# Kernel optimization log

Hardware: AMD Instinct MI355X
Metric: run time of the kernel (lower is better)

Reference implementation:

```python
import jax, jax.numpy as jnp
import numpy as np

N_NODES = 50000
N_EDGES = 800000
N_GRAPHS = 1024
N_LAYERS = 5
D_IN, D_HID = 32, 128


def setup_inputs() -> dict:
    key = jax.random.key(0)
    ks = jax.random.split(key, 6)
    x = jax.random.normal(ks[0], (N_NODES, D_IN), dtype=jnp.float32)
    edge_index = jax.random.randint(ks[1], (2, N_EDGES), 0, N_NODES, dtype=jnp.int64)
    batch = jnp.sort(jax.random.randint(ks[2], (N_NODES,), 0, N_GRAPHS, dtype=jnp.int64))
    W_embed = jax.random.normal(ks[3], (D_IN, D_HID), dtype=jnp.float32) * (1.0 / np.sqrt(D_IN))
    Ws = jax.random.normal(ks[4], (N_LAYERS, D_HID, D_HID), dtype=jnp.float32) * (1.0 / np.sqrt(D_HID))
    bs = jax.random.normal(ks[5], (N_LAYERS, D_HID), dtype=jnp.float32) * 0.01
    return {"x": x, "edge_index": edge_index, "batch": batch,
            "W_embed": W_embed, "Ws": Ws, "bs": bs}


def reference(x, edge_index, batch, W_embed, Ws, bs):
    src, dst = edge_index[0], edge_index[1]
    h = x @ W_embed  # [N, 128] embedding (bias=False)
    features = [h]
    for i in range(N_LAYERS):
        # GINConv with eps=0 and explicit self-loops:
        # agg = sum_{j in N(i)} h_j + h_i (self-loop); out = Linear((1+eps)*h_i + agg)
        neigh = jax.ops.segment_sum(h[src], dst, num_segments=N_NODES)
        agg = neigh + 2.0 * h  # self-loop contribution + (1+eps)*h, eps=0
        h = agg @ Ws[i] + bs[i]
        features.append(h)
    node_repr = jnp.concatenate(features, axis=-1)  # [N, 6*128]
    graph_repr = jax.ops.segment_sum(node_repr, batch, num_segments=N_GRAPHS)  # [G, 768]
    return graph_repr
```

## Files before the change

kernel.cpp:

```cpp
#include <hip/hip_runtime.h>

#define N_NODES 50000
#define N_EDGES 800000
#define N_GRAPHS 1024
#define N_LAYERS 5
#define D_IN 32
#define D_HID 128

#define NBUCK 256
#define BUCK_NODES 196
#define BUCK_CAP 4096
#define CHUNK 4096
#define NCHUNKS ((N_EDGES + CHUNK - 1) / CHUNK)

typedef __attribute__((ext_vector_type(8))) short bf16x8;
typedef __attribute__((ext_vector_type(4))) float f32x4;


__device__ __forceinline__ float bf_lo(unsigned u) { return __uint_as_float(u << 16); }
__device__ __forceinline__ float bf_hi(unsigned u) { return __uint_as_float(u & 0xffff0000u); }
__device__ __forceinline__ unsigned bf16_rn(float f) {
  unsigned u = __float_as_uint(f);
  return (u + 0x7fffu + ((u >> 16) & 1u)) >> 16;
}
__device__ __forceinline__ unsigned pack_bf16(float a, float b) {
  return bf16_rn(a) | (bf16_rn(b) << 16);
}


__global__ void zero_int_kernel(int* __restrict__ p, int n) {
  int i = blockIdx.x * blockDim.x + threadIdx.x;
  if (i < n) p[i] = 0;
}

__global__ __launch_bounds__(256) void bucket_count_kernel(const int* __restrict__ dst,
                                                           int* __restrict__ bcount) {
  __shared__ int cnt[NBUCK];
  for (int i = threadIdx.x; i < NBUCK; i += 256) cnt[i] = 0;
  __syncthreads();
  const int cb = blockIdx.x * CHUNK;
  const int end = (cb + CHUNK < N_EDGES) ? cb + CHUNK : N_EDGES;
  for (int e = cb + threadIdx.x; e < end; e += 256)
    atomicAdd(&cnt[dst[e] / BUCK_NODES], 1);
  __syncthreads();
  for (int i = threadIdx.x; i < NBUCK; i += 256)
    if (cnt[i]) atomicAdd(&bcount[i], cnt[i]);
}

__global__ __launch_bounds__(256) void bucket_scan_kernel(const int* __restrict__ bcount,
                                                          int* __restrict__ bbase,
                                                          int* __restrict__ gcur) {
  __shared__ int s[NBUCK];
  const int t = threadIdx.x;
  const int v0 = bcount[t];
  s[t] = v0;
  __syncthreads();
  #pragma unroll
  for (int d = 1; d < NBUCK; d <<= 1) {
    int v = (t >= d) ? s[t - d] : 0;
    __syncthreads();
    s[t] += v;
    __syncthreads();
  }
  bbase[t + 1] = s[t];
  if (t == 0) bbase[0] = 0;
  gcur[t] = s[t] - v0;
}

__global__ __launch_bounds__(256) void bucket_scatter_kernel(const int* __restrict__ src,
                                                             const int* __restrict__ dst,
                                                             int* __restrict__ gcur,
                                                             unsigned long long* __restrict__ aux) {
  __shared__ int cnt[NBUCK];
  __shared__ int base_[NBUCK];
  __shared__ int cur[NBUCK];
  for (int i = threadIdx.x; i < NBUCK; i += 256) cnt[i] = 0;
  __syncthreads();
  const int cb = blockIdx.x * CHUNK;
  const int end = (cb + CHUNK < N_EDGES) ? cb + CHUNK : N_EDGES;
  for (int e = cb + threadIdx.x; e < end; e += 256)
    atomicAdd(&cnt[dst[e] / BUCK_NODES], 1);
  __syncthreads();
  for (int i = threadIdx.x; i < NBUCK; i += 256) {
    base_[i] = cnt[i] ? atomicAdd(&gcur[i], cnt[i]) : 0;
    cur[i] = 0;
  }
  __syncthreads();
  for (int e = cb + threadIdx.x; e < end; e += 256) {
    const int d = dst[e];
    const int b = d / BUCK_NODES;
    const int p = base_[b] + atomicAdd(&cur[b], 1);
    aux[p] = ((unsigned long long)(unsigned)d << 32) | (unsigned)src[e];
  }
}

__global__ __launch_bounds__(256) void bucket_csr_kernel(const unsigned long long* __restrict__ aux,
                                                         const int* __restrict__ bbase,
                                                         int* __restrict__ off,
                                                         int* __restrict__ csr) {
  __shared__ int sdeg[NBUCK];
  __shared__ int sscan[NBUCK];
  __shared__ int scur[NBUCK];
  __shared__ int lcsr[BUCK_CAP];
  const int b = blockIdx.x, t = threadIdx.x;
  const int e0 = bbase[b], e1 = bbase[b + 1];
  const int n0 = b * BUCK_NODES;
  const int nN = (N_NODES - n0 < BUCK_NODES) ? (N_NODES - n0) : BUCK_NODES;
  sdeg[t] = 0;
  __syncthreads();
  for (int i = e0 + t; i < e1; i += 256)
    atomicAdd(&sdeg[(int)(aux[i] >> 32) - n0], 1);
  __syncthreads();
  sscan[t] = sdeg[t];
  __syncthreads();
  #pragma unroll
  for (int d = 1; d < NBUCK; d <<= 1) {
    int v = (t >= d) ? sscan[t - d] : 0;
    __syncthreads();
    sscan[t] += v;
    __syncthreads();
  }
  const int exc_t = sscan[t] - sdeg[t];
  __syncthreads();
  sscan[t] = exc_t;
  scur[t] = 0;
  if (t < nN) off[n0 + t] = e0 + exc_t;
  if (b == NBUCK - 1 && t == 0) off[N_NODES] = e1;
  __syncthreads();
  for (int i = e0 + t; i < e1; i += 256) {
    const unsigned long long v = aux[i];
    const int d = (int)(v >> 32) - n0;
    const int pos = sscan[d] + atomicAdd(&scur[d], 1);
    const int s = (int)(unsigned)(v & 0xffffffffu);
    if (pos < BUCK_CAP) lcsr[pos] = s;
    else csr[e0 + pos] = s;
  }
  __syncthreads();
  const int cntAll = e1 - e0;
  const int lim = (cntAll < BUCK_CAP) ? cntAll : BUCK_CAP;
  for (int i = t; i < lim; i += 256) csr[e0 + i] = lcsr[i];
}

__global__ void graph_off_kernel(const int* __restrict__ batch, int* __restrict__ goff) {
  int g = blockIdx.x * blockDim.x + threadIdx.x;
  if (g <= N_GRAPHS) {
    int lo = 0, hi = N_NODES;
    while (lo < hi) { int mid = (lo + hi) >> 1; if (batch[mid] < g) lo = mid + 1; else hi = mid; }
    goff[g] = lo;
  }
}

__global__ void pack_w_kernel(const float* __restrict__ Ws,
                              unsigned short* __restrict__ wb_hi,
                              unsigned short* __restrict__ wb_lo) {
  int idx = blockIdx.x * blockDim.x + threadIdx.x;
  if (idx >= N_LAYERS * 16384) return;
  int layer = idx >> 14;
  int r = idx & 16383;
  int t = r >> 9;
  int lane = (r >> 3) & 63;
  int i = r & 7;
  int nt = t >> 2, kt = t & 3;
  int k = kt * 32 + (lane >> 4) * 8 + i;
  int c = nt * 16 + (lane & 15);
  float f = Ws[(size_t)layer * 16384 + k * D_HID + c];
  unsigned short h = (unsigned short)bf16_rn(f);
  float hf = __uint_as_float(((unsigned)h) << 16);
  unsigned short l = (unsigned short)bf16_rn(f - hf);
  wb_hi[idx] = h;
  wb_lo[idx] = l;
}


__global__ __launch_bounds__(256) void embed_kernel(const float* __restrict__ x,
                                                    const float* __restrict__ W,
                                                    unsigned short* __restrict__ hb) {
  __shared__ float Wl[D_IN * D_HID];
  __shared__ float xl[64 * D_IN];
  for (int i = threadIdx.x; i < D_IN * D_HID; i += 256) Wl[i] = W[i];
  const int base = blockIdx.x * 64;
  const int nThis = (base + 64 <= N_NODES) ? 64 : (N_NODES - base);
  const float4* x4 = reinterpret_cast<const float4*>(x + (size_t)base * D_IN);
  for (int i = threadIdx.x; i < nThis * (D_IN / 4); i += 256)
    reinterpret_cast<float4*>(xl)[i] = x4[i];
  __syncthreads();
  const int c2 = (threadIdx.x & 63) * 2;
  const int sub = threadIdx.x >> 6;
  for (int r = sub; r < nThis; r += 4) {
    float s0 = 0.f, s1 = 0.f;
    #pragma unroll
    for (int k = 0; k < D_IN; ++k) {
      float xv = xl[r * D_IN + k];
      s0 += xv * Wl[k * D_HID + c2];
      s1 += xv * Wl[k * D_HID + c2 + 1];
    }
    *reinterpret_cast<unsigned*>(hb + (size_t)(base + r) * D_HID + c2) = pack_bf16(s0, s1);
  }
}

__global__ __launch_bounds__(256, 6) void gin_layer_kernel(const unsigned short* __restrict__ hb,
                                                           const int* __restrict__ off,
                                                           const int* __restrict__ csr,
                                                           const unsigned short* __restrict__ wb_hi,
                                                           const unsigned short* __restrict__ wb_lo,
                                                           const float* __restrict__ b,
                                                           unsigned short* __restrict__ hbout) {
  __shared__ unsigned atile[16 * 64];
  const int wid = threadIdx.x >> 6;
  const int lane = threadIdx.x & 63;
  const int base_m = blockIdx.x * 16;
  const int q = lane >> 4;
  const int l16 = lane & 15;
  const int r = wid * 4 + q;
  const int node = base_m + r;

  const int e0 = off[node], e1 = off[node + 1];
  const int deg = e1 - e0;

  float s[8];
  {
    const uint4 su = *reinterpret_cast<const uint4*>(hb + (size_t)node * D_HID + l16 * 8);
    const unsigned* sw = reinterpret_cast<const unsigned*>(&su);
    #pragma unroll
    for (int i = 0; i < 4; ++i) {
      s[2 * i]     = 2.f * bf_lo(sw[i]);
      s[2 * i + 1] = 2.f * bf_hi(sw[i]);
    }
  }

  for (int bb = 0; bb < deg; bb += 16) {
    const int epos = e0 + bb + l16;
    const int vidx = (epos < e1) ? csr[epos] : 0;
    #pragma unroll
    for (int half = 0; half < 2; ++half) {
      const int jb = half * 8;
      if (bb + jb < deg) {
        uint4 u[8];
        #pragma unroll
        for (int j = 0; j < 8; ++j) {
          const int idx = __shfl(vidx, (lane & 48) + jb + j, 64);
          u[j] = *reinterpret_cast<const uint4*>(hb + (size_t)idx * D_HID + l16 * 8);
        }
        const int rem = deg - bb - jb;
        #pragma unroll
        for (int j = 0; j < 8; ++j) {
          const float sc = (j < rem) ? 1.f : 0.f;
          const unsigned* uw = reinterpret_cast<const unsigned*>(&u[j]);
          #pragma unroll
          for (int i = 0; i < 4; ++i) {
            s[2 * i]     += sc * bf_lo(uw[i]);
            s[2 * i + 1] += sc * bf_hi(uw[i]);
          }
        }
      }
    }
  }

  {
    uint4 pk;
    unsigned* pw = reinterpret_cast<unsigned*>(&pk);
    #pragma unroll
    for (int i = 0; i < 4; ++i) pw[i] = pack_bf16(s[2 * i], s[2 * i + 1]);
    const int wbase = (l16 * 4) ^ ((r & 7) << 2);
    *reinterpret_cast<uint4*>(&atile[r * 64 + wbase]) = pk;
  }
  __syncthreads();

  const int l15 = lane & 15;
  const int lg = lane >> 4;
  bf16x8 a[4];
  #pragma unroll
  for (int kt = 0; kt < 4; ++kt) {
    const int u32off = l15 * 64 + ((kt * 16 + lg * 4) ^ ((l15 & 7) << 2));
    a[kt] = *reinterpret_cast<const bf16x8*>(&atile[u32off]);
  }
  #pragma unroll
  for (int qq = 0; qq < 2; ++qq) {
    const int nt = wid * 2 + qq;
    f32x4 acc = {0.f, 0.f, 0.f, 0.f};
    #pragma unroll
    for (int kt = 0; kt < 4; ++kt) {
      const int toff = (nt * 4 + kt) * 512 + lane * 8;
      bf16x8 bh = *reinterpret_cast<const bf16x8*>(wb_hi + toff);
      bf16x8 bl = *reinterpret_cast<const bf16x8*>(wb_lo + toff);
      acc = __builtin_amdgcn_mfma_f32_16x16x32_bf16(a[kt], bh, acc, 0, 0, 0);
      acc = __builtin_amdgcn_mfma_f32_16x16x32_bf16(a[kt], bl, acc, 0, 0, 0);
    }
    const int col = nt * 16 + l15;
    const float bcol = b[col];
    #pragma unroll
    for (int i = 0; i < 4; ++i) {
      const int onode = base_m + lg * 4 + i;
      hbout[(size_t)onode * D_HID + col] = (unsigned short)bf16_rn(acc[i] + bcol);
    }
  }
}

__global__ __launch_bounds__(256) void pool6_kernel(const unsigned short* __restrict__ h0,
                                                    const unsigned short* __restrict__ h1,
                                                    const unsigned short* __restrict__ h2,
                                                    const unsigned short* __restrict__ h3,
                                                    const unsigned short* __restrict__ h4,
                                                    const unsigned short* __restrict__ h5,
                                                    const int* __restrict__ goff,
                                                    float* __restrict__ out) {
  const int g = blockIdx.x * 8 + (threadIdx.x >> 5);
  const int t = threadIdx.x & 31;
  if (g >= N_GRAPHS) return;
  const int n0 = goff[g], n1 = goff[g + 1];
  float4 s0 = {0,0,0,0}, s1 = {0,0,0,0}, s2 = {0,0,0,0};
  float4 s3 = {0,0,0,0}, s4 = {0,0,0,0}, s5 = {0,0,0,0};
  for (int n = n0; n < n1; ++n) {
    const size_t o = (size_t)n * D_HID + t * 4;
    uint2 v0 = *reinterpret_cast<const uint2*>(h0 + o);
    uint2 v1 = *reinterpret_cast<const uint2*>(h1 + o);
    uint2 v2 = *reinterpret_cast<const uint2*>(h2 + o);
    uint2 v3 = *reinterpret_cast<const uint2*>(h3 + o);
    uint2 v4 = *reinterpret_cast<const uint2*>(h4 + o);
    uint2 v5 = *reinterpret_cast<const uint2*>(h5 + o);
    s0.x += bf_lo(v0.x); s0.y += bf_hi(v0.x); s0.z += bf_lo(v0.y); s0.w += bf_hi(v0.y);
    s1.x += bf_lo(v1.x); s1.y += bf_hi(v1.x); s1.z += bf_lo(v1.y); s1.w += bf_hi(v1.y);
    s2.x += bf_lo(v2.x); s2.y += bf_hi(v2.x); s2.z += bf_lo(v2.y); s2.w += bf_hi(v2.y);
    s3.x += bf_lo(v3.x); s3.y += bf_hi(v3.x); s3.z += bf_lo(v3.y); s3.w += bf_hi(v3.y);
    s4.x += bf_lo(v4.x); s4.y += bf_hi(v4.x); s4.z += bf_lo(v4.y); s4.w += bf_hi(v4.y);
    s5.x += bf_lo(v5.x); s5.y += bf_hi(v5.x); s5.z += bf_lo(v5.y); s5.w += bf_hi(v5.y);
  }
  float* ob = out + (size_t)g * ((N_LAYERS + 1) * D_HID) + t * 4;
  *reinterpret_cast<float4*>(ob + 0 * D_HID) = s0;
  *reinterpret_cast<float4*>(ob + 1 * D_HID) = s1;
  *reinterpret_cast<float4*>(ob + 2 * D_HID) = s2;
  *reinterpret_cast<float4*>(ob + 3 * D_HID) = s3;
  *reinterpret_cast<float4*>(ob + 4 * D_HID) = s4;
  *reinterpret_cast<float4*>(ob + 5 * D_HID) = s5;
}


extern "C" void kernel_launch(void* const* d_in, const int* in_sizes, int n_in,
                              void* d_out, int out_size, void* d_ws, size_t ws_size,
                              hipStream_t stream) {
  const float* x       = (const float*)d_in[0];
  const int*   edges   = (const int*)d_in[1];
  const int*   src     = edges;
  const int*   dst     = edges + N_EDGES;
  const int*   batch   = (const int*)d_in[2];
  const float* W_embed = (const float*)d_in[3];
  const float* Ws      = (const float*)d_in[4];
  const float* bs      = (const float*)d_in[5];
  float* out = (float*)d_out;

  const size_t HSZ = (size_t)N_NODES * D_HID;
  unsigned short* hb[N_LAYERS + 1];
  hb[0] = (unsigned short*)d_ws;
  for (int l = 1; l <= N_LAYERS; ++l) hb[l] = hb[l - 1] + HSZ;
  unsigned short* wb_hi = hb[N_LAYERS] + HSZ;
  unsigned short* wb_lo = wb_hi + (size_t)N_LAYERS * 16384;
  unsigned long long* aux = (unsigned long long*)(wb_lo + (size_t)N_LAYERS * 16384);
  int*   off    = (int*)(aux + N_EDGES);
  int*   bcount = off + (N_NODES + 1);
  int*   bbase  = bcount + NBUCK;
  int*   gcur   = bbase + (NBUCK + 1);
  int*   csr    = gcur + NBUCK;
  int*   goff   = csr + N_EDGES;

  zero_int_kernel<<<1, 256, 0, stream>>>(bcount, NBUCK);
  bucket_count_kernel<<<NCHUNKS, 256, 0, stream>>>(dst, bcount);
  bucket_scan_kernel<<<1, NBUCK, 0, stream>>>(bcount, bbase, gcur);
  bucket_scatter_kernel<<<NCHUNKS, 256, 0, stream>>>(src, dst, gcur, aux);
  bucket_csr_kernel<<<NBUCK, 256, 0, stream>>>(aux, bbase, off, csr);
  graph_off_kernel<<<(N_GRAPHS + 1 + 255) / 256, 256, 0, stream>>>(batch, goff);

  pack_w_kernel<<<(N_LAYERS * 16384 + 255) / 256, 256, 0, stream>>>(Ws, wb_hi, wb_lo);

  embed_kernel<<<(N_NODES + 63) / 64, 256, 0, stream>>>(x, W_embed, hb[0]);

  for (int l = 0; l < N_LAYERS; ++l) {
    gin_layer_kernel<<<N_NODES / 16, 256, 0, stream>>>(hb[l], off, csr,
                                                       wb_hi + (size_t)l * 16384,
                                                       wb_lo + (size_t)l * 16384,
                                                       bs + (size_t)l * D_HID, hb[l + 1]);
  }

  pool6_kernel<<<N_GRAPHS / 8, 256, 0, stream>>>(hb[0], hb[1], hb[2], hb[3], hb[4], hb[5],
                                                 goff, out);
}
```

Before: 269.1 us.

## Fuse pooling into layer epilogues via atomics and drop CSR count/scan passes

```diff
diff --git a/kernel.cpp b/kernel.cpp
--- a/kernel.cpp
+++ b/kernel.cpp
@@ -6,10 +6,11 @@
 #define N_LAYERS 5
 #define D_IN 32
 #define D_HID 128
+#define OUT_COLS ((N_LAYERS + 1) * D_HID)
 
 #define NBUCK 256
 #define BUCK_NODES 196
-#define BUCK_CAP 4096
+#define BUCK_REG 8192
 #define CHUNK 4096
 #define NCHUNKS ((N_EDGES + CHUNK - 1) / CHUNK)
 
@@ -27,45 +28,6 @@
   return bf16_rn(a) | (bf16_rn(b) << 16);
 }
 
-
-__global__ void zero_int_kernel(int* __restrict__ p, int n) {
-  int i = blockIdx.x * blockDim.x + threadIdx.x;
-  if (i < n) p[i] = 0;
-}
-
-__global__ __launch_bounds__(256) void bucket_count_kernel(const int* __restrict__ dst,
-                                                           int* __restrict__ bcount) {
-  __shared__ int cnt[NBUCK];
-  for (int i = threadIdx.x; i < NBUCK; i += 256) cnt[i] = 0;
-  __syncthreads();
-  const int cb = blockIdx.x * CHUNK;
-  const int end = (cb + CHUNK < N_EDGES) ? cb + CHUNK : N_EDGES;
-  for (int e = cb + threadIdx.x; e < end; e += 256)
-    atomicAdd(&cnt[dst[e] / BUCK_NODES], 1);
-  __syncthreads();
-  for (int i = threadIdx.x; i < NBUCK; i += 256)
-    if (cnt[i]) atomicAdd(&bcount[i], cnt[i]);
-}
-
-__global__ __launch_bounds__(256) void bucket_scan_kernel(const int* __restrict__ bcount,
-                                                          int* __restrict__ bbase,
-                                                          int* __restrict__ gcur) {
-  __shared__ int s[NBUCK];
-  const int t = threadIdx.x;
-  const int v0 = bcount[t];
-  s[t] = v0;
-  __syncthreads();
-  #pragma unroll
-  for (int d = 1; d < NBUCK; d <<= 1) {
-    int v = (t >= d) ? s[t - d] : 0;
-    __syncthreads();
-    s[t] += v;
-    __syncthreads();
-  }
-  bbase[t + 1] = s[t];
-  if (t == 0) bbase[0] = 0;
-  gcur[t] = s[t] - v0;
-}
 
 __global__ __launch_bounds__(256) void bucket_scatter_kernel(const int* __restrict__ src,
                                                              const int* __restrict__ dst,
@@ -90,26 +52,51 @@
     const int d = dst[e];
     const int b = d / BUCK_NODES;
     const int p = base_[b] + atomicAdd(&cur[b], 1);
-    aux[p] = ((unsigned long long)(unsigned)d << 32) | (unsigned)src[e];
-  }
-}
-
-__global__ __launch_bounds__(256) void bucket_csr_kernel(const unsigned long long* __restrict__ aux,
-                                                         const int* __restrict__ bbase,
-                                                         int* __restrict__ off,
-                                                         int* __restrict__ csr) {
+    if (p < BUCK_REG)
+      aux[(size_t)b * BUCK_REG + p] = ((unsigned long long)(unsigned)d << 32) | (unsigned)src[e];
+  }
+}
+
+__global__ __launch_bounds__(256) void csr_packw_kernel(const unsigned long long* __restrict__ aux,
+                                                        const int* __restrict__ gcur,
+                                                        int* __restrict__ off,
+                                                        int* __restrict__ deg,
+                                                        int* __restrict__ csr,
+                                                        const float* __restrict__ Ws,
+                                                        unsigned short* __restrict__ wb_hi,
+                                                        unsigned short* __restrict__ wb_lo) {
+  if (blockIdx.x >= NBUCK) {
+    const int idx = (blockIdx.x - NBUCK) * 256 + threadIdx.x;
+    if (idx < N_LAYERS * 16384) {
+      const int layer = idx >> 14;
+      const int r = idx & 16383;
+      const int t = r >> 9;
+      const int lane = (r >> 3) & 63;
+      const int i = r & 7;
+      const int nt = t >> 2, kt = t & 3;
+      const int k = kt * 32 + (lane >> 4) * 8 + i;
+      const int c = nt * 16 + (lane & 15);
+      const float f = Ws[(size_t)layer * 16384 + k * D_HID + c];
+      const unsigned short h = (unsigned short)bf16_rn(f);
+      const float hf = __uint_as_float(((unsigned)h) << 16);
+      wb_hi[idx] = h;
+      wb_lo[idx] = (unsigned short)bf16_rn(f - hf);
+    }
+    return;
+  }
   __shared__ int sdeg[NBUCK];
   __shared__ int sscan[NBUCK];
   __shared__ int scur[NBUCK];
-  __shared__ int lcsr[BUCK_CAP];
+  __shared__ int lcsr[BUCK_REG];
   const int b = blockIdx.x, t = threadIdx.x;
-  const int e0 = bbase[b], e1 = bbase[b + 1];
+  const int abase = b * BUCK_REG;
+  int cnt = gcur[b]; if (cnt > BUCK_REG) cnt = BUCK_REG;
   const int n0 = b * BUCK_NODES;
   const int nN = (N_NODES - n0 < BUCK_NODES) ? (N_NODES - n0) : BUCK_NODES;
   sdeg[t] = 0;
   __syncthreads();
-  for (int i = e0 + t; i < e1; i += 256)
-    atomicAdd(&sdeg[(int)(aux[i] >> 32) - n0], 1);
+  for (int i = t; i < cnt; i += 256)
+    atomicAdd(&sdeg[(int)(aux[(size_t)abase + i] >> 32) - n0], 1);
   __syncthreads();
   sscan[t] = sdeg[t];
   __syncthreads();
@@ -124,57 +111,24 @@
   __syncthreads();
   sscan[t] = exc_t;
   scur[t] = 0;
-  if (t < nN) off[n0 + t] = e0 + exc_t;
-  if (b == NBUCK - 1 && t == 0) off[N_NODES] = e1;
-  __syncthreads();
-  for (int i = e0 + t; i < e1; i += 256) {
-    const unsigned long long v = aux[i];
+  if (t < nN) { off[n0 + t] = abase + exc_t; deg[n0 + t] = sdeg[t]; }
+  __syncthreads();
+  for (int i = t; i < cnt; i += 256) {
+    const unsigned long long v = aux[(size_t)abase + i];
     const int d = (int)(v >> 32) - n0;
     const int pos = sscan[d] + atomicAdd(&scur[d], 1);
-    const int s = (int)(unsigned)(v & 0xffffffffu);
-    if (pos < BUCK_CAP) lcsr[pos] = s;
-    else csr[e0 + pos] = s;
-  }
-  __syncthreads();
-  const int cntAll = e1 - e0;
-  const int lim = (cntAll < BUCK_CAP) ? cntAll : BUCK_CAP;
-  for (int i = t; i < lim; i += 256) csr[e0 + i] = lcsr[i];
-}
-
-__global__ void graph_off_kernel(const int* __restrict__ batch, int* __restrict__ goff) {
-  int g = blockIdx.x * blockDim.x + threadIdx.x;
-  if (g <= N_GRAPHS) {
-    int lo = 0, hi = N_NODES;
-    while (lo < hi) { int mid = (lo + hi) >> 1; if (batch[mid] < g) lo = mid + 1; else hi = mid; }
-    goff[g] = lo;
-  }
-}
-
-__global__ void pack_w_kernel(const float* __restrict__ Ws,
-                              unsigned short* __restrict__ wb_hi,
-                              unsigned short* __restrict__ wb_lo) {
-  int idx = blockIdx.x * blockDim.x + threadIdx.x;
-  if (idx >= N_LAYERS * 16384) return;
-  int layer = idx >> 14;
-  int r = idx & 16383;
-  int t = r >> 9;
-  int lane = (r >> 3) & 63;
-  int i = r & 7;
-  int nt = t >> 2, kt = t & 3;
-  int k = kt * 32 + (lane >> 4) * 8 + i;
-  int c = nt * 16 + (lane & 15);
-  float f = Ws[(size_t)layer * 16384 + k * D_HID + c];
-  unsigned short h = (unsigned short)bf16_rn(f);
-  float hf = __uint_as_float(((unsigned)h) << 16);
-  unsigned short l = (unsigned short)bf16_rn(f - hf);
-  wb_hi[idx] = h;
-  wb_lo[idx] = l;
+    lcsr[pos] = (int)(unsigned)(v & 0xffffffffu);
+  }
+  __syncthreads();
+  for (int i = t; i < cnt; i += 256) csr[abase + i] = lcsr[i];
 }
 
 
 __global__ __launch_bounds__(256) void embed_kernel(const float* __restrict__ x,
                                                     const float* __restrict__ W,
-                                                    unsigned short* __restrict__ hb) {
+                                                    const int* __restrict__ batch,
+                                                    unsigned short* __restrict__ hb,
+                                                    float* __restrict__ out) {
   __shared__ float Wl[D_IN * D_HID];
   __shared__ float xl[64 * D_IN];
   for (int i = threadIdx.x; i < D_IN * D_HID; i += 256) Wl[i] = W[i];
@@ -195,16 +149,22 @@
       s1 += xv * Wl[k * D_HID + c2 + 1];
     }
     *reinterpret_cast<unsigned*>(hb + (size_t)(base + r) * D_HID + c2) = pack_bf16(s0, s1);
+    const int g = batch[base + r];
+    atomicAdd(out + (size_t)g * OUT_COLS + c2, s0);
+    atomicAdd(out + (size_t)g * OUT_COLS + c2 + 1, s1);
   }
 }
 
 __global__ __launch_bounds__(256, 6) void gin_layer_kernel(const unsigned short* __restrict__ hb,
                                                            const int* __restrict__ off,
+                                                           const int* __restrict__ degarr,
                                                            const int* __restrict__ csr,
                                                            const unsigned short* __restrict__ wb_hi,
                                                            const unsigned short* __restrict__ wb_lo,
                                                            const float* __restrict__ b,
-                                                           unsigned short* __restrict__ hbout) {
+                                                           const int* __restrict__ batch,
+                                                           unsigned short* __restrict__ hbout,
+                                                           float* __restrict__ out, int lslice) {
   __shared__ unsigned atile[16 * 64];
   const int wid = threadIdx.x >> 6;
   const int lane = threadIdx.x & 63;
@@ -214,8 +174,8 @@
   const int r = wid * 4 + q;
   const int node = base_m + r;
 
-  const int e0 = off[node], e1 = off[node + 1];
-  const int deg = e1 - e0;
+  const int e0 = off[node];
+  const int deg = degarr[node];
 
   float s[8];
   {
@@ -229,8 +189,7 @@
   }
 
   for (int bb = 0; bb < deg; bb += 16) {
-    const int epos = e0 + bb + l16;
-    const int vidx = (epos < e1) ? csr[epos] : 0;
+    const int vidx = (bb + l16 < deg) ? csr[e0 + bb + l16] : 0;
     #pragma unroll
     for (int half = 0; half < 2; ++half) {
       const int jb = half * 8;
@@ -291,47 +250,12 @@
     #pragma unroll
     for (int i = 0; i < 4; ++i) {
       const int onode = base_m + lg * 4 + i;
-      hbout[(size_t)onode * D_HID + col] = (unsigned short)bf16_rn(acc[i] + bcol);
-    }
-  }
-}
-
-__global__ __launch_bounds__(256) void pool6_kernel(const unsigned short* __restrict__ h0,
-                                                    const unsigned short* __restrict__ h1,
-                                                    const unsigned short* __restrict__ h2,
-                                                    const unsigned short* __restrict__ h3,
-                                                    const unsigned short* __restrict__ h4,
-                                                    const unsigned short* __restrict__ h5,
-                                                    const int* __restrict__ goff,
-                                                    float* __restrict__ out) {
-  const int g = blockIdx.x * 8 + (threadIdx.x >> 5);
-  const int t = threadIdx.x & 31;
-  if (g >= N_GRAPHS) return;
-  const int n0 = goff[g], n1 = goff[g + 1];
-  float4 s0 = {0,0,0,0}, s1 = {0,0,0,0}, s2 = {0,0,0,0};
-  float4 s3 = {0,0,0,0}, s4 = {0,0,0,0}, s5 = {0,0,0,0};
-  for (int n = n0; n < n1; ++n) {
-    const size_t o = (size_t)n * D_HID + t * 4;
-    uint2 v0 = *reinterpret_cast<const uint2*>(h0 + o);
-    uint2 v1 = *reinterpret_cast<const uint2*>(h1 + o);
-    uint2 v2 = *reinterpret_cast<const uint2*>(h2 + o);
-    uint2 v3 = *reinterpret_cast<const uint2*>(h3 + o);
-    uint2 v4 = *reinterpret_cast<const uint2*>(h4 + o);
-    uint2 v5 = *reinterpret_cast<const uint2*>(h5 + o);
-    s0.x += bf_lo(v0.x); s0.y += bf_hi(v0.x); s0.z += bf_lo(v0.y); s0.w += bf_hi(v0.y);
-    s1.x += bf_lo(v1.x); s1.y += bf_hi(v1.x); s1.z += bf_lo(v1.y); s1.w += bf_hi(v1.y);
-    s2.x += bf_lo(v2.x); s2.y += bf_hi(v2.x); s2.z += bf_lo(v2.y); s2.w += bf_hi(v2.y);
-    s3.x += bf_lo(v3.x); s3.y += bf_hi(v3.x); s3.z += bf_lo(v3.y); s3.w += bf_hi(v3.y);
-    s4.x += bf_lo(v4.x); s4.y += bf_hi(v4.x); s4.z += bf_lo(v4.y); s4.w += bf_hi(v4.y);
-    s5.x += bf_lo(v5.x); s5.y += bf_hi(v5.x); s5.z += bf_lo(v5.y); s5.w += bf_hi(v5.y);
-  }
-  float* ob = out + (size_t)g * ((N_LAYERS + 1) * D_HID) + t * 4;
-  *reinterpret_cast<float4*>(ob + 0 * D_HID) = s0;
-  *reinterpret_cast<float4*>(ob + 1 * D_HID) = s1;
-  *reinterpret_cast<float4*>(ob + 2 * D_HID) = s2;
-  *reinterpret_cast<float4*>(ob + 3 * D_HID) = s3;
-  *reinterpret_cast<float4*>(ob + 4 * D_HID) = s4;
-  *reinterpret_cast<float4*>(ob + 5 * D_HID) = s5;
+      const float v = acc[i] + bcol;
+      hbout[(size_t)onode * D_HID + col] = (unsigned short)bf16_rn(v);
+      const int g = batch[onode];
+      atomicAdd(out + (size_t)g * OUT_COLS + lslice + col, v);
+    }
+  }
 }
 
 
@@ -355,31 +279,26 @@
   unsigned short* wb_hi = hb[N_LAYERS] + HSZ;
   unsigned short* wb_lo = wb_hi + (size_t)N_LAYERS * 16384;
   unsigned long long* aux = (unsigned long long*)(wb_lo + (size_t)N_LAYERS * 16384);
-  int*   off    = (int*)(aux + N_EDGES);
-  int*   bcount = off + (N_NODES + 1);
-  int*   bbase  = bcount + NBUCK;
-  int*   gcur   = bbase + (NBUCK + 1);
-  int*   csr    = gcur + NBUCK;
-  int*   goff   = csr + N_EDGES;
-
-  zero_int_kernel<<<1, 256, 0, stream>>>(bcount, NBUCK);
-  bucket_count_kernel<<<NCHUNKS, 256, 0, stream>>>(dst, bcount);
-  bucket_scan_kernel<<<1, NBUCK, 0, stream>>>(bcount, bbase, gcur);
+  int* csr  = (int*)(aux + (size_t)NBUCK * BUCK_REG);
+  int* off  = csr + (size_t)NBUCK * BUCK_REG;
+  int* deg  = off + N_NODES;
+  int* gcur = deg + N_NODES;
+
+  hipMemsetAsync(gcur, 0, NBUCK * sizeof(int), stream);
+  hipMemsetAsync(out, 0, (size_t)out_size * sizeof(float), stream);
+
   bucket_scatter_kernel<<<NCHUNKS, 256, 0, stream>>>(src, dst, gcur, aux);
-  bucket_csr_kernel<<<NBUCK, 256, 0, stream>>>(aux, bbase, off, csr);
-  graph_off_kernel<<<(N_GRAPHS + 1 + 255) / 256, 256, 0, stream>>>(batch, goff);
-
-  pack_w_kernel<<<(N_LAYERS * 16384 + 255) / 256, 256, 0, stream>>>(Ws, wb_hi, wb_lo);
-
-  embed_kernel<<<(N_NODES + 63) / 64, 256, 0, stream>>>(x, W_embed, hb[0]);
+  csr_packw_kernel<<<NBUCK + (N_LAYERS * 16384 + 255) / 256, 256, 0, stream>>>(
+      aux, gcur, off, deg, csr, Ws, wb_hi, wb_lo);
+
+  embed_kernel<<<(N_NODES + 63) / 64, 256, 0, stream>>>(x, W_embed, batch, hb[0], out);
 
   for (int l = 0; l < N_LAYERS; ++l) {
-    gin_layer_kernel<<<N_NODES / 16, 256, 0, stream>>>(hb[l], off, csr,
+    gin_layer_kernel<<<N_NODES / 16, 256, 0, stream>>>(hb[l], off, deg, csr,
                                                        wb_hi + (size_t)l * 16384,
                                                        wb_lo + (size_t)l * 16384,
-                                                       bs + (size_t)l * D_HID, hb[l + 1]);
-  }
-
-  pool6_kernel<<<N_GRAPHS / 8, 256, 0, stream>>>(hb[0], hb[1], hb[2], hb[3], hb[4], hb[5],
-                                                 goff, out);
-}
+                                                       bs + (size_t)l * D_HID,
+                                                       batch, hb[l + 1],
+                                                       out, (l + 1) * D_HID);
+  }
+}
```

New measurement: 654.3 us. +143.2%, slower.
